# Optimization experiments

Measured on AMD Instinct MI355X. Metric: run time of the kernel, lower is better.

## Reference

```python
import jax, jax.numpy as jnp
import numpy as np

USER_NUM, ITEM_NUM, EMB, R = 8192, 16384, 32, 3

def setup_inputs() -> dict:
    key = jax.random.key(0)
    k1, k2, k3 = jax.random.split(key, 3)
    # Xavier-uniform-like embeddings
    u_lim = (6.0 / (USER_NUM + EMB)) ** 0.5
    i_lim = (6.0 / (ITEM_NUM + EMB)) ** 0.5
    user_emb = jax.random.uniform(k1, (USER_NUM, EMB), jnp.float32, -u_lim, u_lim)
    item_emb = jax.random.uniform(k2, (ITEM_NUM, EMB), jnp.float32, -i_lim, i_lim)
    # Densified normalized link-propagation matrix (user x item).
    # Scale ~1/item_num so repeated propagation stays numerically tame,
    # mimicking the degree-normalized product in __init__.
    sparse_norm = jax.random.uniform(k3, (USER_NUM, ITEM_NUM), jnp.float32) * (2.0 / ITEM_NUM)
    return {"user_emb": user_emb, "item_emb": item_emb, "sparse_norm": sparse_norm}

def reference(user_emb, item_emb, sparse_norm):
    # LinkProp forward (t == 0.0 branch): r rounds of cross propagation,
    # then mean over the (r+1) layer outputs. Running sums avoid stacking.
    u_k, i_k = user_emb, item_emb
    u_sum, i_sum = user_emb, item_emb
    for _ in range(R):
        u_next = sparse_norm @ i_k          # [U, d]
        i_next = sparse_norm.T @ u_k        # [I, d]
        u_sum = u_sum + u_next
        i_sum = i_sum + i_next
        u_k, i_k = u_next, i_next
    inv = 1.0 / (R + 1)
    return (u_sum * inv, i_sum * inv)
```

## Files before the change

kernel.cpp:

```cpp
#include <hip/hip_runtime.h>

#define U_N 8192
#define I_N 16384

typedef float f4 __attribute__((ext_vector_type(4)));
typedef unsigned long long u64;

__device__ __forceinline__ unsigned char f2e4m3(float x) {
  unsigned char sign = (x < 0.f) ? 0x80 : 0x00;
  float ax = fabsf(x);
  unsigned char code;
  if (ax >= 448.f) {
    code = 0x7E;
  } else if (ax < 0.015625f) {
    int q = (int)rintf(ax * 512.f);
    code = (unsigned char)q;
  } else {
    int e; float f = frexpf(ax, &e);
    int q = (int)rintf(f * 16.f);
    if (q == 16) { q = 8; e += 1; }
    code = (unsigned char)(((e + 6) << 3) | (q - 8));
  }
  return sign | code;
}

#define SCALE_S   131072.f
#define SCALE_V0  512.f
#define SCALE_VK  65536.f

__global__ __launch_bounds__(256)
void convert_kernel(const float* __restrict__ Sf,
                    const float* __restrict__ u0,
                    const float* __restrict__ i0,
                    unsigned char* __restrict__ S8,
                    unsigned char* __restrict__ wT0,
                    unsigned char* __restrict__ vT0)
{
  const int tid = threadIdx.x;
  const int bid = blockIdx.x;
  if (bid < 1024) {
    const int idx = bid * 256 + tid;
    wT0[(idx & 31) * U_N + (idx >> 5)] = f2e4m3(u0[idx] * SCALE_V0);
  } else if (bid < 3072) {
    const int idx = (bid - 1024) * 256 + tid;
    vT0[(idx & 31) * I_N + (idx >> 5)] = f2e4m3(i0[idx] * SCALE_V0);
  } else {
    const size_t base = (size_t)(bid - 3072) * 4096 + (size_t)tid * 16;
    const float4* src = (const float4*)(Sf + base);
    union { unsigned char b[16]; uint4 v; } out;
#pragma unroll
    for (int g = 0; g < 4; ++g) {
      float4 f = src[g];
      out.b[g * 4 + 0] = f2e4m3(f.x * SCALE_S);
      out.b[g * 4 + 1] = f2e4m3(f.y * SCALE_S);
      out.b[g * 4 + 2] = f2e4m3(f.z * SCALE_S);
      out.b[g * 4 + 3] = f2e4m3(f.w * SCALE_S);
    }
    *(uint4*)&S8[base] = out.v;
  }
}

template <bool F8>
__global__ __launch_bounds__(256, 4)
void pass_kernel(const unsigned char* __restrict__ S8,
                 const float* __restrict__ Sf,
                 const unsigned char* __restrict__ vT,
                 const unsigned char* __restrict__ wT,
                 float* __restrict__ u_part,
                 float* __restrict__ i_part,
                 float descale)
{
  __shared__ unsigned char smem[16896];
  const int tid = threadIdx.x;
  const int lane = tid & 63;
  const int wave = tid >> 6;
  const int m = lane & 15;
  const int quad = lane >> 4;
  const int bid = blockIdx.x;

  if (bid < 1024) {
    const int rg = bid & 127, ks = bid >> 7;
    const int r0 = rg * 64 + wave * 16;
    const int cbase = ks * 2048;
    f4 acc0 = {0.f, 0.f, 0.f, 0.f};
    f4 acc1 = {0.f, 0.f, 0.f, 0.f};
    for (int ch = 0; ch < 4; ++ch) {
      const int cb = cbase + ch * 512;
#pragma unroll
      for (int it = 0; it < 4; ++it) {
        const int idx = it * 256 + tid;
        const int e = idx >> 5;
        const int o = (idx & 31) * 16;
        *(uint4*)&smem[e * 528 + o] = *(const uint4*)&vT[(size_t)e * I_N + cb + o];
      }
      __syncthreads();
#pragma unroll
      for (int kk = 0; kk < 512; kk += 32) {
        long a;
        if (F8) {
          a = *(const long*)(S8 + (size_t)(r0 + m) * I_N + cb + kk + quad * 8);
        } else {
          const float* p = Sf + (size_t)(r0 + m) * I_N + cb + kk + quad * 8;
          u64 av = 0;
#pragma unroll
          for (int j = 0; j < 8; ++j) av |= (u64)f2e4m3(p[j] * SCALE_S) << (8 * j);
          a = (long)av;
        }
        const long b0 = *(const long*)&smem[m * 528 + kk + quad * 8];
        const long b1 = *(const long*)&smem[(m + 16) * 528 + kk + quad * 8];
        acc0 = __builtin_amdgcn_mfma_f32_16x16x32_fp8_fp8(a, b0, acc0, 0, 0, 0);
        acc1 = __builtin_amdgcn_mfma_f32_16x16x32_fp8_fp8(a, b1, acc1, 0, 0, 0);
      }
      __syncthreads();
    }
    float* dst = u_part + (size_t)ks * (U_N * 32);
#pragma unroll
    for (int i2 = 0; i2 < 4; ++i2) {
      const int r = r0 + quad * 4 + i2;
      dst[r * 32 + m]      = acc0[i2] * descale;
      dst[r * 32 + 16 + m] = acc1[i2] * descale;
    }
  } else {
    const int b = bid - 1024;
    const int cg = b & 255, rs = b >> 8;
    const int c0 = cg * 64;
    const int rbase = rs * 2048;
    const int cw = wave * 16;
    unsigned char* stile = smem;
    unsigned char* wlds  = smem + 9216;
    f4 acc0 = {0.f, 0.f, 0.f, 0.f};
    f4 acc1 = {0.f, 0.f, 0.f, 0.f};
    for (int ch = 0; ch < 16; ++ch) {
      const int rb = rbase + ch * 128;
#pragma unroll
      for (int it = 0; it < 4; ++it) {
        const int idx = it * 256 + tid;
        const int rr = idx >> 3;
        const int o = (idx & 7) * 8;
        if (F8) {
          *(u64*)&stile[rr * 72 + o] =
              *(const u64*)(S8 + (size_t)(rb + rr) * I_N + c0 + o);
        } else {
          const float* p = Sf + (size_t)(rb + rr) * I_N + c0 + o;
          u64 v = 0;
#pragma unroll
          for (int j = 0; j < 8; ++j) v |= (u64)f2e4m3(p[j] * SCALE_S) << (8 * j);
          *(u64*)&stile[rr * 72 + o] = v;
        }
      }
      {
        const int e = tid >> 3;
        const int o = (tid & 7) * 16;
        *(uint4*)&wlds[e * 144 + o] = *(const uint4*)&wT[(size_t)e * U_N + rb + o];
      }
      __syncthreads();
#pragma unroll
      for (int kk = 0; kk < 128; kk += 32) {
        u64 av = 0;
#pragma unroll
        for (int j = 0; j < 8; ++j)
          av |= (u64)stile[(kk + quad * 8 + j) * 72 + cw + m] << (8 * j);
        const long b0 = *(const long*)&wlds[m * 144 + kk + quad * 8];
        const long b1 = *(const long*)&wlds[(m + 16) * 144 + kk + quad * 8];
        acc0 = __builtin_amdgcn_mfma_f32_16x16x32_fp8_fp8((long)av, b0, acc0, 0, 0, 0);
        acc1 = __builtin_amdgcn_mfma_f32_16x16x32_fp8_fp8((long)av, b1, acc1, 0, 0, 0);
      }
      __syncthreads();
    }
    float* dst = i_part + (size_t)rs * (I_N * 32);
#pragma unroll
    for (int i2 = 0; i2 < 4; ++i2) {
      const int c = c0 + cw + quad * 4 + i2;
      dst[c * 32 + m]      = acc0[i2] * descale;
      dst[c * 32 + 16 + m] = acc1[i2] * descale;
    }
  }
}

__global__ __launch_bounds__(256)
void reduce_kernel(const float* __restrict__ u_part, const float* __restrict__ i_part,
                   const float* __restrict__ u0, const float* __restrict__ i0,
                   float* __restrict__ acc_u, float* __restrict__ acc_i,
                   unsigned char* __restrict__ wT, unsigned char* __restrict__ vT,
                   float* __restrict__ out_u, float* __restrict__ out_i,
                   int round)
{
  const int gid = blockIdx.x * 256 + threadIdx.x;
  if (gid < U_N * 32) {
    float s = 0.f;
#pragma unroll
    for (int sp = 0; sp < 8; ++sp) s += u_part[(size_t)sp * (U_N * 32) + gid];
    if (round == 1)      acc_u[gid] = u0[gid] + s;
    else if (round == 2) acc_u[gid] += s;
    else                 out_u[gid] = (acc_u[gid] + s) * 0.25f;
    if (round < 3) wT[(gid & 31) * U_N + (gid >> 5)] = f2e4m3(s * SCALE_VK);
  } else {
    const int g = gid - U_N * 32;
    float s = 0.f;
#pragma unroll
    for (int sp = 0; sp < 4; ++sp) s += i_part[(size_t)sp * (I_N * 32) + g];
    if (round == 1)      acc_i[g] = i0[g] + s;
    else if (round == 2) acc_i[g] += s;
    else                 out_i[g] = (acc_i[g] + s) * 0.25f;
    if (round < 3) vT[(g & 31) * I_N + (g >> 5)] = f2e4m3(s * SCALE_VK);
  }
}

extern "C" void kernel_launch(void* const* d_in, const int* in_sizes, int n_in,
                              void* d_out, int out_size, void* d_ws, size_t ws_size,
                              hipStream_t stream) {
  const float* u0 = (const float*)d_in[0];
  const float* i0 = (const float*)d_in[1];
  const float* Sf = (const float*)d_in[2];
  float* out_u = (float*)d_out;
  float* out_i = out_u + U_N * 32;
  unsigned char* ws = (unsigned char*)d_ws;

  const size_t S8_BYTES = (size_t)U_N * I_N;
  const size_t SMALL_BYTES = 20709376;
  const bool f8 = ws_size >= S8_BYTES + SMALL_BYTES;

  unsigned char* S8;
  unsigned char* cur;
  if (f8) { S8 = ws; cur = ws + S8_BYTES; }
  else    { S8 = nullptr; cur = ws; }
  float* u_part = (float*)cur;
  float* i_part = u_part + 8 * U_N * 32;
  float* acc_u  = i_part + 4 * I_N * 32;
  float* acc_i  = acc_u + U_N * 32;
  unsigned char* wT = (unsigned char*)(acc_i + I_N * 32);
  unsigned char* vT = wT + 32 * U_N;

  convert_kernel<<<f8 ? 35840 : 3072, 256, 0, stream>>>(Sf, u0, i0, S8, wT, vT);

  const float ds1 = 1.f / (SCALE_S * SCALE_V0);
  const float dsk = 1.f / (SCALE_S * SCALE_VK);
  for (int round = 1; round <= 3; ++round) {
    const float ds = (round == 1) ? ds1 : dsk;
    if (f8)
      pass_kernel<true><<<2048, 256, 0, stream>>>(S8, nullptr, vT, wT, u_part, i_part, ds);
    else
      pass_kernel<false><<<2048, 256, 0, stream>>>(nullptr, Sf, vT, wT, u_part, i_part, ds);
    reduce_kernel<<<3072, 256, 0, stream>>>(u_part, i_part, u0, i0, acc_u, acc_i,
                                            wT, vT, out_u, out_i, round);
  }
}
```

Measured before the change: 943.2 us.

## Precompute transposed FP8 matrix and use hardware FP8 conversion

The convert kernel now writes a second FP8 copy of the propagation matrix, transposed through an LDS tile. The item-side pass can then reuse the same row-major MFMA routine as the user side instead of gathering bytes from LDS one at a time. Software float-to-e4m3 conversion is replaced with the packed hardware conversion builtin when the compiler provides it. The cost is an extra 128 MB write in the convert step and double the workspace requirement. If the workspace is too small, every pass falls back to converting the fp32 matrix on the fly, which is much slower.

```diff
diff --git a/kernel.cpp b/kernel.cpp
--- a/kernel.cpp
+++ b/kernel.cpp
@@ -6,7 +6,16 @@
 typedef float f4 __attribute__((ext_vector_type(4)));
 typedef unsigned long long u64;
 
-__device__ __forceinline__ unsigned char f2e4m3(float x) {
+#if defined(__has_builtin)
+#if __has_builtin(__builtin_amdgcn_cvt_pk_fp8_f32)
+#define HAS_HW_FP8 1
+#endif
+#endif
+#ifndef HAS_HW_FP8
+#define HAS_HW_FP8 0
+#endif
+
+__device__ __forceinline__ unsigned char f2e4m3_soft(float x) {
   unsigned char sign = (x < 0.f) ? 0x80 : 0x00;
   float ax = fabsf(x);
   unsigned char code;
@@ -24,6 +33,25 @@
   return sign | code;
 }
 
+__device__ __forceinline__ unsigned char q8(float x) {
+#if HAS_HW_FP8
+  return (unsigned char)(__builtin_amdgcn_cvt_pk_fp8_f32(x, 0.f, 0, false) & 0xff);
+#else
+  return f2e4m3_soft(x);
+#endif
+}
+
+__device__ __forceinline__ unsigned int pack4_fp8(float a, float b, float c, float d) {
+#if HAS_HW_FP8
+  int v = __builtin_amdgcn_cvt_pk_fp8_f32(a, b, 0, false);
+  v = __builtin_amdgcn_cvt_pk_fp8_f32(c, d, v, true);
+  return (unsigned int)v;
+#else
+  return (unsigned)f2e4m3_soft(a) | ((unsigned)f2e4m3_soft(b) << 8) |
+         ((unsigned)f2e4m3_soft(c) << 16) | ((unsigned)f2e4m3_soft(d) << 24);
+#endif
+}
+
 #define SCALE_S   131072.f
 #define SCALE_V0  512.f
 #define SCALE_VK  65536.f
@@ -33,6 +61,7 @@
                     const float* __restrict__ u0,
                     const float* __restrict__ i0,
                     unsigned char* __restrict__ S8,
+                    unsigned char* __restrict__ S8T,
                     unsigned char* __restrict__ wT0,
                     unsigned char* __restrict__ vT0)
 {
@@ -40,35 +69,117 @@
   const int bid = blockIdx.x;
   if (bid < 1024) {
     const int idx = bid * 256 + tid;
-    wT0[(idx & 31) * U_N + (idx >> 5)] = f2e4m3(u0[idx] * SCALE_V0);
+    wT0[(idx & 31) * U_N + (idx >> 5)] = q8(u0[idx] * SCALE_V0);
   } else if (bid < 3072) {
     const int idx = (bid - 1024) * 256 + tid;
-    vT0[(idx & 31) * I_N + (idx >> 5)] = f2e4m3(i0[idx] * SCALE_V0);
-  } else {
-    const size_t base = (size_t)(bid - 3072) * 4096 + (size_t)tid * 16;
-    const float4* src = (const float4*)(Sf + base);
-    union { unsigned char b[16]; uint4 v; } out;
-#pragma unroll
-    for (int g = 0; g < 4; ++g) {
-      float4 f = src[g];
-      out.b[g * 4 + 0] = f2e4m3(f.x * SCALE_S);
-      out.b[g * 4 + 1] = f2e4m3(f.y * SCALE_S);
-      out.b[g * 4 + 2] = f2e4m3(f.z * SCALE_S);
-      out.b[g * 4 + 3] = f2e4m3(f.w * SCALE_S);
-    }
-    *(uint4*)&S8[base] = out.v;
-  }
-}
-
-template <bool F8>
+    vT0[(idx & 31) * I_N + (idx >> 5)] = q8(i0[idx] * SCALE_V0);
+  } else {
+    __shared__ unsigned char lds[64 * 68];
+    const int b = bid - 3072;
+    const int tr = b >> 8;
+    const int tc = b & 255;
+    const int mr = (tid >> 4) << 2;
+    const int mc = (tid & 15) << 2;
+    const size_t base = ((size_t)tr * 64 + mr) * I_N + (size_t)tc * 64 + mc;
+    float fs[4][4];
+#pragma unroll
+    for (int i = 0; i < 4; ++i) {
+      float4 f = *(const float4*)(Sf + base + (size_t)i * I_N);
+      fs[i][0] = f.x * SCALE_S; fs[i][1] = f.y * SCALE_S;
+      fs[i][2] = f.z * SCALE_S; fs[i][3] = f.w * SCALE_S;
+    }
+#pragma unroll
+    for (int i = 0; i < 4; ++i)
+      *(unsigned int*)&S8[base + (size_t)i * I_N] =
+          pack4_fp8(fs[i][0], fs[i][1], fs[i][2], fs[i][3]);
+#pragma unroll
+    for (int j = 0; j < 4; ++j)
+      *(unsigned int*)&lds[(mc + j) * 68 + mr] =
+          pack4_fp8(fs[0][j], fs[1][j], fs[2][j], fs[3][j]);
+    __syncthreads();
+    const int c = tid >> 2;
+    const int s = (tid & 3) << 4;
+    uint4 v;
+    v.x = *(const unsigned int*)&lds[c * 68 + s];
+    v.y = *(const unsigned int*)&lds[c * 68 + s + 4];
+    v.z = *(const unsigned int*)&lds[c * 68 + s + 8];
+    v.w = *(const unsigned int*)&lds[c * 68 + s + 12];
+    *(uint4*)&S8T[((size_t)tc * 64 + c) * U_N + (size_t)tr * 64 + s] = v;
+  }
+}
+
+__device__ __forceinline__ void half_gemm(
+    const unsigned char* __restrict__ A,
+    const unsigned char* __restrict__ Bt,
+    float* __restrict__ part,
+    unsigned char* smem,
+    int rgroup, int ksplit, int nrows, size_t kdim, float descale, int tid)
+{
+  const int lane = tid & 63;
+  const int wave = tid >> 6;
+  const int m = lane & 15;
+  const int quad = lane >> 4;
+  const int r0 = rgroup * 64 + wave * 16;
+  const int kbase = ksplit * 2048;
+  f4 acc0 = {0.f, 0.f, 0.f, 0.f};
+  f4 acc1 = {0.f, 0.f, 0.f, 0.f};
+  for (int ch = 0; ch < 4; ++ch) {
+    const int kb = kbase + ch * 512;
+#pragma unroll
+    for (int it = 0; it < 4; ++it) {
+      const int idx = it * 256 + tid;
+      const int e = idx >> 5;
+      const int o = (idx & 31) * 16;
+      *(uint4*)&smem[e * 528 + o] = *(const uint4*)&Bt[(size_t)e * kdim + kb + o];
+    }
+    __syncthreads();
+#pragma unroll
+    for (int kk = 0; kk < 512; kk += 32) {
+      const long a  = *(const long*)(A + (size_t)(r0 + m) * kdim + kb + kk + quad * 8);
+      const long b0 = *(const long*)&smem[m * 528 + kk + quad * 8];
+      const long b1 = *(const long*)&smem[(m + 16) * 528 + kk + quad * 8];
+      acc0 = __builtin_amdgcn_mfma_f32_16x16x32_fp8_fp8(a, b0, acc0, 0, 0, 0);
+      acc1 = __builtin_amdgcn_mfma_f32_16x16x32_fp8_fp8(a, b1, acc1, 0, 0, 0);
+    }
+    __syncthreads();
+  }
+  float* dst = part + (size_t)ksplit * ((size_t)nrows * 32);
+#pragma unroll
+  for (int i2 = 0; i2 < 4; ++i2) {
+    const int r = r0 + quad * 4 + i2;
+    dst[r * 32 + m]      = acc0[i2] * descale;
+    dst[r * 32 + 16 + m] = acc1[i2] * descale;
+  }
+}
+
 __global__ __launch_bounds__(256, 4)
 void pass_kernel(const unsigned char* __restrict__ S8,
-                 const float* __restrict__ Sf,
+                 const unsigned char* __restrict__ S8T,
                  const unsigned char* __restrict__ vT,
                  const unsigned char* __restrict__ wT,
                  float* __restrict__ u_part,
                  float* __restrict__ i_part,
                  float descale)
+{
+  __shared__ unsigned char smem[16896];
+  const int bid = blockIdx.x;
+  if (bid < 1024) {
+    half_gemm(S8, vT, u_part, smem, bid & 127, bid >> 7, U_N, (size_t)I_N,
+              descale, threadIdx.x);
+  } else {
+    const int b = bid - 1024;
+    half_gemm(S8T, wT, i_part, smem, b & 255, b >> 8, I_N, (size_t)U_N,
+              descale, threadIdx.x);
+  }
+}
+
+__global__ __launch_bounds__(256, 4)
+void pass_fallback(const float* __restrict__ Sf,
+                   const unsigned char* __restrict__ vT,
+                   const unsigned char* __restrict__ wT,
+                   float* __restrict__ u_part,
+                   float* __restrict__ i_part,
+                   float descale)
 {
   __shared__ unsigned char smem[16896];
   const int tid = threadIdx.x;
@@ -96,16 +207,11 @@
       __syncthreads();
 #pragma unroll
       for (int kk = 0; kk < 512; kk += 32) {
-        long a;
-        if (F8) {
-          a = *(const long*)(S8 + (size_t)(r0 + m) * I_N + cb + kk + quad * 8);
-        } else {
-          const float* p = Sf + (size_t)(r0 + m) * I_N + cb + kk + quad * 8;
-          u64 av = 0;
-#pragma unroll
-          for (int j = 0; j < 8; ++j) av |= (u64)f2e4m3(p[j] * SCALE_S) << (8 * j);
-          a = (long)av;
-        }
+        const float* p = Sf + (size_t)(r0 + m) * I_N + cb + kk + quad * 8;
+        u64 av = 0;
+#pragma unroll
+        for (int j = 0; j < 8; ++j) av |= (u64)q8(p[j] * SCALE_S) << (8 * j);
+        const long a = (long)av;
         const long b0 = *(const long*)&smem[m * 528 + kk + quad * 8];
         const long b1 = *(const long*)&smem[(m + 16) * 528 + kk + quad * 8];
         acc0 = __builtin_amdgcn_mfma_f32_16x16x32_fp8_fp8(a, b0, acc0, 0, 0, 0);
@@ -137,16 +243,11 @@
         const int idx = it * 256 + tid;
         const int rr = idx >> 3;
         const int o = (idx & 7) * 8;
-        if (F8) {
-          *(u64*)&stile[rr * 72 + o] =
-              *(const u64*)(S8 + (size_t)(rb + rr) * I_N + c0 + o);
-        } else {
-          const float* p = Sf + (size_t)(rb + rr) * I_N + c0 + o;
-          u64 v = 0;
-#pragma unroll
-          for (int j = 0; j < 8; ++j) v |= (u64)f2e4m3(p[j] * SCALE_S) << (8 * j);
-          *(u64*)&stile[rr * 72 + o] = v;
-        }
+        const float* p = Sf + (size_t)(rb + rr) * I_N + c0 + o;
+        u64 v = 0;
+#pragma unroll
+        for (int j = 0; j < 8; ++j) v |= (u64)q8(p[j] * SCALE_S) << (8 * j);
+        *(u64*)&stile[rr * 72 + o] = v;
       }
       {
         const int e = tid >> 3;
@@ -193,7 +294,7 @@
     if (round == 1)      acc_u[gid] = u0[gid] + s;
     else if (round == 2) acc_u[gid] += s;
     else                 out_u[gid] = (acc_u[gid] + s) * 0.25f;
-    if (round < 3) wT[(gid & 31) * U_N + (gid >> 5)] = f2e4m3(s * SCALE_VK);
+    if (round < 3) wT[(gid & 31) * U_N + (gid >> 5)] = q8(s * SCALE_VK);
   } else {
     const int g = gid - U_N * 32;
     float s = 0.f;
@@ -202,7 +303,7 @@
     if (round == 1)      acc_i[g] = i0[g] + s;
     else if (round == 2) acc_i[g] += s;
     else                 out_i[g] = (acc_i[g] + s) * 0.25f;
-    if (round < 3) vT[(g & 31) * I_N + (g >> 5)] = f2e4m3(s * SCALE_VK);
+    if (round < 3) vT[(g & 31) * I_N + (g >> 5)] = q8(s * SCALE_VK);
   }
 }
 
@@ -218,12 +319,13 @@
 
   const size_t S8_BYTES = (size_t)U_N * I_N;
   const size_t SMALL_BYTES = 20709376;
-  const bool f8 = ws_size >= S8_BYTES + SMALL_BYTES;
-
-  unsigned char* S8;
+  const bool f8 = ws_size >= 2 * S8_BYTES + SMALL_BYTES;
+
+  unsigned char* S8 = nullptr;
+  unsigned char* S8T = nullptr;
   unsigned char* cur;
-  if (f8) { S8 = ws; cur = ws + S8_BYTES; }
-  else    { S8 = nullptr; cur = ws; }
+  if (f8) { S8 = ws; S8T = ws + S8_BYTES; cur = ws + 2 * S8_BYTES; }
+  else    { cur = ws; }
   float* u_part = (float*)cur;
   float* i_part = u_part + 8 * U_N * 32;
   float* acc_u  = i_part + 4 * I_N * 32;
@@ -231,16 +333,16 @@
   unsigned char* wT = (unsigned char*)(acc_i + I_N * 32);
   unsigned char* vT = wT + 32 * U_N;
 
-  convert_kernel<<<f8 ? 35840 : 3072, 256, 0, stream>>>(Sf, u0, i0, S8, wT, vT);
+  convert_kernel<<<f8 ? 35840 : 3072, 256, 0, stream>>>(Sf, u0, i0, S8, S8T, wT, vT);
 
   const float ds1 = 1.f / (SCALE_S * SCALE_V0);
   const float dsk = 1.f / (SCALE_S * SCALE_VK);
   for (int round = 1; round <= 3; ++round) {
     const float ds = (round == 1) ? ds1 : dsk;
     if (f8)
-      pass_kernel<true><<<2048, 256, 0, stream>>>(S8, nullptr, vT, wT, u_part, i_part, ds);
+      pass_kernel<<<2048, 256, 0, stream>>>(S8, S8T, vT, wT, u_part, i_part, ds);
     else
-      pass_kernel<false><<<2048, 256, 0, stream>>>(nullptr, Sf, vT, wT, u_part, i_part, ds);
+      pass_fallback<<<2048, 256, 0, stream>>>(Sf, vT, wT, u_part, i_part, ds);
     reduce_kernel<<<3072, 256, 0, stream>>>(u_part, i_part, u0, i0, acc_u, acc_i,
                                             wT, vT, out_u, out_i, round);
   }
```

Result: slower. 1.014 ms (+7.6%).
